# Kernel tuning notes

Measured on AMD Instinct MI355X. Metric: run time of the kernel, lower is better.

## Reference

```python
import jax, jax.numpy as jnp
import numpy as np

N, D, E, H, K = 16384, 256, 8, 512, 2


def setup_inputs() -> dict:
    key = jax.random.key(0)
    ks = jax.random.split(key, 5)
    inputs = jax.random.normal(ks[0], (N, D), dtype=jnp.float32)
    Wg = jax.random.normal(ks[1], (D, E), dtype=jnp.float32) * 0.05
    w1 = jax.random.normal(ks[2], (E, D, H), dtype=jnp.float32) * 0.05
    b1 = jnp.zeros((E, H), dtype=jnp.float32)
    w2 = jax.random.normal(ks[3], (E, H, D), dtype=jnp.float32) * 0.05
    b2 = jnp.zeros((E, D), dtype=jnp.float32)
    return {"inputs": inputs, "Wg": Wg, "w1": w1, "b1": b1, "w2": w2, "b2": b2}


def reference(inputs, Wg, w1, b1, w2, b2):
    # gate + top-k routing (softmax over the selected logits only, as in the torch code)
    gate_logits = inputs @ Wg                       # [N, E]
    topw, topi = jax.lax.top_k(gate_logits, K)      # [N, K]
    topw = jax.nn.softmax(topw.astype(jnp.float32), axis=1).astype(inputs.dtype)
    # combine weights scattered back into a dense [N, E] matrix (dispatch/combine)
    combine = jnp.zeros((N, E), dtype=inputs.dtype)
    combine = combine.at[jnp.arange(N)[:, None], topi].add(topw)  # [N, E]
    # expert MLP (Linear -> GELU(exact) -> Linear), computed per expert and
    # combined with the sparse routing weights (pool='sum')
    h = jax.nn.gelu(jnp.einsum('nd,edh->neh', inputs, w1) + b1[None], approximate=False)  # [N,E,H]
    y = jnp.einsum('neh,ehd->ned', h, w2) + b2[None]                                      # [N,E,D]
    return jnp.einsum('ne,ned->nd', combine, y)                                           # [N,D]
```

## Files before the change

### kernel.cpp

```cpp
#include <hip/hip_runtime.h>

#define NTOK 16384
#define DIM 256
#define NEXP 8
#define HID 512
#define CAP 5120
#define CSTRIDE 16

typedef unsigned short ushort_t;
typedef short bf16x8 __attribute__((ext_vector_type(8)));
typedef float f32x4 __attribute__((ext_vector_type(4)));

static __device__ __forceinline__ ushort_t f2bf(float f) {
    unsigned int u = __float_as_uint(f);
    unsigned int r = (u + 0x7FFFu + ((u >> 16) & 1u)) >> 16;
    return (ushort_t)r;
}
static __device__ __forceinline__ float bf2f(ushort_t u) {
    unsigned int x = ((unsigned int)u) << 16;
    return __uint_as_float(x);
}
static __device__ __forceinline__ float gelu_fast(float v) {
    float v2 = v * v;
    float u = v * __builtin_fmaf(v2, -0.1029407079f, -2.3022090196f);
    float e = __builtin_amdgcn_exp2f(u);
    return v * __builtin_amdgcn_rcpf(1.0f + e);
}

__global__ void k_prep(const float* __restrict__ X, const float* __restrict__ Wg,
                       const float* __restrict__ w1, const float* __restrict__ w2,
                       int* counts, int* tok_list, int* inv_idx, float* inv_w,
                       ushort_t* __restrict__ Xb,
                       ushort_t* __restrict__ w1t, ushort_t* __restrict__ w2t) {
    __shared__ __align__(16) char smem[69504];
    int tid = threadIdx.x;
    if (blockIdx.x >= 256) {
        ushort_t (*tile)[72] = (ushort_t(*)[72])smem;
        int b = blockIdx.x - 256;
        const float* src; ushort_t* dst; int R, C, e, t;
        if (b < 256) { e = b >> 5; t = b & 31; src = w1; dst = w1t + e * DIM * HID; R = DIM; C = HID; }
        else { b -= 256; e = b >> 5; t = b & 31; src = w2; dst = w2t + e * DIM * HID; R = HID; C = DIM; }
        size_t ebase = (size_t)e * DIM * HID;
        int tilesC = C >> 6;
        int rt = t / tilesC, ct = t % tilesC;
        for (int i = 0; i < 16; i++) {
            int flat = i * 256 + tid;
            int lr = flat >> 6, lc = flat & 63;
            tile[lr][lc] = f2bf(src[ebase + (size_t)(rt * 64 + lr) * C + ct * 64 + lc]);
        }
        __syncthreads();
        for (int i = 0; i < 16; i++) {
            int flat = i * 256 + tid;
            int lr = flat >> 6, lc = flat & 63;
            dst[(ct * 64 + lr) * R + rt * 64 + lc] = tile[lc][lr];
        }
        return;
    }
    float (*xs)[257] = (float(*)[257])smem;
    float (*lg)[8] = (float(*)[8])(smem + 65792);
    int* te0 = (int*)(smem + 67840);
    int* te1 = (int*)(smem + 68096);
    int* lo0 = (int*)(smem + 68352);
    int* lo1 = (int*)(smem + 68608);
    float* tw0 = (float*)(smem + 68864);
    float* tw1 = (float*)(smem + 69120);
    int* lcnt = (int*)(smem + 69376);
    int* gbase = (int*)(smem + 69408);
    int tok0 = blockIdx.x * 64;
    if (tid < NEXP) lcnt[tid] = 0;
    for (int i = 0; i < 8; i++) {
        int flat = i * 256 + tid;
        int r = flat >> 5, c8 = (flat & 31) << 3;
        const float* row = X + (size_t)(tok0 + r) * DIM + c8;
        float4 a = *(const float4*)row;
        float4 b = *(const float4*)(row + 4);
        xs[r][c8 + 0] = a.x; xs[r][c8 + 1] = a.y; xs[r][c8 + 2] = a.z; xs[r][c8 + 3] = a.w;
        xs[r][c8 + 4] = b.x; xs[r][c8 + 5] = b.y; xs[r][c8 + 6] = b.z; xs[r][c8 + 7] = b.w;
    }
    __syncthreads();
    for (int i = 0; i < 8; i++) {
        int flat = i * 256 + tid;
        int r = flat >> 5, c8 = (flat & 31) << 3;
        ushort_t pk[8];
#pragma unroll
        for (int j = 0; j < 8; j++) pk[j] = f2bf(xs[r][c8 + j]);
        *(int4*)(Xb + (size_t)(tok0 + r) * DIM + c8) = *(const int4*)pk;
    }
    int tl = tid & 63, pair = tid >> 6;
    float l0 = 0.f, l1 = 0.f;
    for (int d = 0; d < DIM; d++) {
        float x = xs[tl][d];
        l0 += x * Wg[d * NEXP + 2 * pair];
        l1 += x * Wg[d * NEXP + 2 * pair + 1];
    }
    lg[tl][2 * pair] = l0; lg[tl][2 * pair + 1] = l1;
    __syncthreads();
    if (tid < 64) {
        float best = -1e30f; int bi = 0;
#pragma unroll
        for (int e = 0; e < NEXP; e++) { float v = lg[tid][e]; if (v > best) { best = v; bi = e; } }
        float best2 = -1e30f; int bi2 = 0;
#pragma unroll
        for (int e = 0; e < NEXP; e++) { if (e == bi) continue; float v = lg[tid][e]; if (v > best2) { best2 = v; bi2 = e; } }
        float ed = __expf(best2 - best);
        te0[tid] = bi; te1[tid] = bi2;
        tw0[tid] = 1.0f / (1.0f + ed);
        tw1[tid] = ed / (1.0f + ed);
        lo0[tid] = atomicAdd(&lcnt[bi], 1);
        lo1[tid] = atomicAdd(&lcnt[bi2], 1);
    }
    __syncthreads();
    if (tid < NEXP) gbase[tid] = atomicAdd(&counts[tid * CSTRIDE], lcnt[tid]);
    __syncthreads();
    if (tid < 64) {
        int token = tok0 + tid;
        int e0 = te0[tid], e1 = te1[tid];
        int p0 = gbase[e0] + lo0[tid]; if (p0 >= CAP) p0 = CAP - 1;
        int p1 = gbase[e1] + lo1[tid]; if (p1 >= CAP) p1 = CAP - 1;
        tok_list[e0 * CAP + p0] = token;
        tok_list[e1 * CAP + p1] = token;
        inv_idx[token * 2]     = (e0 << 16) | p0;  inv_w[token * 2]     = tw0[tid];
        inv_idx[token * 2 + 1] = (e1 << 16) | p1;  inv_w[token * 2 + 1] = tw1[tid];
    }
}

__launch_bounds__(512, 4)
__global__ void k_mlp1(const ushort_t* __restrict__ Xb, const ushort_t* __restrict__ w1t,
                       const float* __restrict__ b1,
                       const int* __restrict__ counts, const int* __restrict__ tok_list,
                       ushort_t* __restrict__ hb) {
    __shared__ ushort_t B1[64 * 264];
    int b = blockIdx.x;
    int e = b / 320;
    int rem = b % 320;
    int hq = rem / 40, tile = rem % 40;
    int count = counts[e * CSTRIDE];
    if (count > CAP) count = CAP;
    int t0 = tile * 128;
    if (t0 >= count) return;

    int tid = threadIdx.x;
    int w = tid >> 6, l = tid & 63, ln = l & 15, q = l >> 4;

    const ushort_t* w1te = w1t + (size_t)e * DIM * HID + (size_t)hq * 64 * DIM;
#pragma unroll
    for (int i = 0; i < 4; i++) {
        int flat = i * 512 + tid;
        int hr = flat >> 5, c8 = (flat & 31) << 3;
        *(int4*)(B1 + hr * 264 + c8) = *(const int4*)(w1te + hr * DIM + c8);
    }
    int arow = t0 + 16 * w + ln;
    int ci = (arow < count) ? arow : (count - 1);
    int atok = tok_list[e * CAP + ci];
    const ushort_t* xrow = Xb + (size_t)atok * DIM;
    bf16x8 xf[8];
#pragma unroll
    for (int ks = 0; ks < 8; ks++)
        xf[ks] = *(const bf16x8*)(xrow + ks * 32 + q * 8);
    __syncthreads();

    f32x4 zf = {0.f, 0.f, 0.f, 0.f};
    f32x4 acc[4];
#pragma unroll
    for (int i = 0; i < 4; i++) acc[i] = zf;
#pragma unroll
    for (int ks = 0; ks < 8; ks++) {
        bf16x8 xk = xf[ks];
#pragma unroll
        for (int cf = 0; cf < 4; cf++) {
            bf16x8 wfr = *(const bf16x8*)(B1 + (cf * 16 + ln) * 264 + ks * 32 + q * 8);
            acc[cf] = __builtin_amdgcn_mfma_f32_16x16x32_bf16(wfr, xk, acc[cf], 0, 0, 0);
        }
    }
    size_t hrowbase = ((size_t)e * CAP + t0 + 16 * w + ln) * HID + hq * 64;
#pragma unroll
    for (int cf = 0; cf < 4; cf++) {
        float4 bv = *(const float4*)(b1 + e * HID + hq * 64 + cf * 16 + q * 4);
        ushort4 pk;
        pk.x = f2bf(gelu_fast(acc[cf][0] + bv.x));
        pk.y = f2bf(gelu_fast(acc[cf][1] + bv.y));
        pk.z = f2bf(gelu_fast(acc[cf][2] + bv.z));
        pk.w = f2bf(gelu_fast(acc[cf][3] + bv.w));
        *(ushort4*)(hb + hrowbase + cf * 16 + q * 4) = pk;
    }
}

__launch_bounds__(512, 2)
__global__ void k_mlp2(const ushort_t* __restrict__ hb, const ushort_t* __restrict__ w2t,
                       const float* __restrict__ b2,
                       const int* __restrict__ counts, ushort_t* __restrict__ yb) {
    __shared__ ushort_t B2[64 * 520];
    int b = blockIdx.x;
    int e = b / 160;
    int rem = b % 160;
    int dq = rem / 40, tile = rem % 40;
    int count = counts[e * CSTRIDE];
    if (count > CAP) count = CAP;
    int t0 = tile * 128;
    if (t0 >= count) return;

    int tid = threadIdx.x;
    int w = tid >> 6, l = tid & 63, ln = l & 15, q = l >> 4;

    const ushort_t* w2te = w2t + (size_t)e * DIM * HID + (size_t)dq * 64 * HID;
#pragma unroll
    for (int i = 0; i < 8; i++) {
        int flat = i * 512 + tid;
        int dr = flat >> 6, c8 = (flat & 63) << 3;
        *(int4*)(B2 + dr * 520 + c8) = *(const int4*)(w2te + dr * HID + c8);
    }
    int arow = t0 + 16 * w + ln;
    int ci = (arow < count) ? arow : (count - 1);
    const ushort_t* hrow = hb + ((size_t)e * CAP + ci) * HID;
    bf16x8 af[16];
#pragma unroll
    for (int ks = 0; ks < 16; ks++)
        af[ks] = *(const bf16x8*)(hrow + ks * 32 + q * 8);
    __syncthreads();

    f32x4 zf = {0.f, 0.f, 0.f, 0.f};
    f32x4 acc[4];
#pragma unroll
    for (int i = 0; i < 4; i++) acc[i] = zf;
#pragma unroll
    for (int ks = 0; ks < 16; ks++) {
        bf16x8 hk = af[ks];
#pragma unroll
        for (int cf = 0; cf < 4; cf++) {
            bf16x8 wfr = *(const bf16x8*)(B2 + (cf * 16 + ln) * 520 + ks * 32 + q * 8);
            acc[cf] = __builtin_amdgcn_mfma_f32_16x16x32_bf16(wfr, hk, acc[cf], 0, 0, 0);
        }
    }
    size_t yrowbase = ((size_t)e * CAP + t0 + 16 * w + ln) * DIM + dq * 64;
#pragma unroll
    for (int cf = 0; cf < 4; cf++) {
        float4 bv = *(const float4*)(b2 + e * DIM + dq * 64 + cf * 16 + q * 4);
        ushort4 pk;
        pk.x = f2bf(acc[cf][0] + bv.x);
        pk.y = f2bf(acc[cf][1] + bv.y);
        pk.z = f2bf(acc[cf][2] + bv.z);
        pk.w = f2bf(acc[cf][3] + bv.w);
        *(ushort4*)(yb + yrowbase + cf * 16 + q * 4) = pk;
    }
}

__global__ void k_combine(const ushort_t* __restrict__ yb, const int* __restrict__ inv_idx,
                          const float* __restrict__ inv_w, float* __restrict__ out) {
    int tid = threadIdx.x;
    int n = blockIdx.x * 8 + (tid >> 5);
    int l32 = tid & 31, c8 = l32 << 3;
    int i0 = inv_idx[2 * n], i1 = inv_idx[2 * n + 1];
    float w0 = inv_w[2 * n], w1 = inv_w[2 * n + 1];
    size_t r0 = (size_t)(i0 >> 16) * CAP + (i0 & 0xFFFF);
    size_t r1 = (size_t)(i1 >> 16) * CAP + (i1 & 0xFFFF);
    int4 v0 = *(const int4*)(yb + r0 * DIM + c8);
    int4 v1 = *(const int4*)(yb + r1 * DIM + c8);
    ushort_t* p0 = (ushort_t*)&v0;
    ushort_t* p1 = (ushort_t*)&v1;
    float4 oa, ob;
    oa.x = w0 * bf2f(p0[0]) + w1 * bf2f(p1[0]);
    oa.y = w0 * bf2f(p0[1]) + w1 * bf2f(p1[1]);
    oa.z = w0 * bf2f(p0[2]) + w1 * bf2f(p1[2]);
    oa.w = w0 * bf2f(p0[3]) + w1 * bf2f(p1[3]);
    ob.x = w0 * bf2f(p0[4]) + w1 * bf2f(p1[4]);
    ob.y = w0 * bf2f(p0[5]) + w1 * bf2f(p1[5]);
    ob.z = w0 * bf2f(p0[6]) + w1 * bf2f(p1[6]);
    ob.w = w0 * bf2f(p0[7]) + w1 * bf2f(p1[7]);
    float4* op = (float4*)(out + (size_t)n * DIM + c8);
    op[0] = oa; op[1] = ob;
}

extern "C" void kernel_launch(void* const* d_in, const int* in_sizes, int n_in,
                              void* d_out, int out_size, void* d_ws, size_t ws_size,
                              hipStream_t stream) {
    const float* X  = (const float*)d_in[0];
    const float* Wg = (const float*)d_in[1];
    const float* w1 = (const float*)d_in[2];
    const float* b1 = (const float*)d_in[3];
    const float* w2 = (const float*)d_in[4];
    const float* b2 = (const float*)d_in[5];

    char* ws = (char*)d_ws;
    size_t off = 0;
    int* counts = (int*)(ws + off);        off = 1024;
    int* tok_list = (int*)(ws + off);      off += (size_t)NEXP * CAP * 4;
    int* inv_idx = (int*)(ws + off);       off += (size_t)NTOK * 2 * 4;
    float* inv_w = (float*)(ws + off);     off += (size_t)NTOK * 2 * 4;
    ushort_t* w1t = (ushort_t*)(ws + off); off += (size_t)NEXP * DIM * HID * 2;
    ushort_t* w2t = (ushort_t*)(ws + off); off += (size_t)NEXP * DIM * HID * 2;
    ushort_t* Xb = (ushort_t*)(ws + off);  off += (size_t)NTOK * DIM * 2;
    ushort_t* hb = (ushort_t*)(ws + off);  off += (size_t)NEXP * CAP * HID * 2;
    ushort_t* yb = (ushort_t*)(ws + off);  off += (size_t)NEXP * CAP * DIM * 2;

    hipMemsetAsync(counts, 0, 1024, stream);
    k_prep<<<768, 256, 0, stream>>>(X, Wg, w1, w2, counts, tok_list, inv_idx, inv_w, Xb, w1t, w2t);
    k_mlp1<<<NEXP * 40 * 8, 512, 0, stream>>>(Xb, w1t, b1, counts, tok_list, hb);
    k_mlp2<<<NEXP * 40 * 4, 512, 0, stream>>>(hb, w2t, b2, counts, yb);
    k_combine<<<2048, 256, 0, stream>>>(yb, inv_idx, inv_w, (float*)d_out);
}
```

Measured before the change: 161.1 us.

## Halve block size and give each wave two 16-row token groups in MLP kernels

Both expert MLP kernels now launch 256 threads instead of 512, and each wave computes two 16-token row groups that share every LDS weight fragment load. This halves LDS weight reads per MFMA and doubles per-wave MFMA work. k_mlp2 splits its K loop into two halves so only 16 activation fragments per pass stay live, and both kernels now skip stores for rows beyond count. The costs are more register pressure per wave, fewer waves to cover the cooperative weight loads, and unchanged LDS footprint per block.

```diff
diff --git a/kernel.cpp b/kernel.cpp
--- a/kernel.cpp
+++ b/kernel.cpp
@@ -124,7 +124,7 @@
     }
 }
 
-__launch_bounds__(512, 4)
+__launch_bounds__(256, 4)
 __global__ void k_mlp1(const ushort_t* __restrict__ Xb, const ushort_t* __restrict__ w1t,
                        const float* __restrict__ b1,
                        const int* __restrict__ counts, const int* __restrict__ tok_list,
@@ -144,48 +144,60 @@
 
     const ushort_t* w1te = w1t + (size_t)e * DIM * HID + (size_t)hq * 64 * DIM;
 #pragma unroll
-    for (int i = 0; i < 4; i++) {
-        int flat = i * 512 + tid;
+    for (int i = 0; i < 8; i++) {
+        int flat = i * 256 + tid;
         int hr = flat >> 5, c8 = (flat & 31) << 3;
         *(int4*)(B1 + hr * 264 + c8) = *(const int4*)(w1te + hr * DIM + c8);
     }
-    int arow = t0 + 16 * w + ln;
-    int ci = (arow < count) ? arow : (count - 1);
-    int atok = tok_list[e * CAP + ci];
-    const ushort_t* xrow = Xb + (size_t)atok * DIM;
-    bf16x8 xf[8];
-#pragma unroll
-    for (int ks = 0; ks < 8; ks++)
-        xf[ks] = *(const bf16x8*)(xrow + ks * 32 + q * 8);
+    int arow0 = t0 + 32 * w + ln;
+    int arow1 = arow0 + 16;
+    int ci0 = (arow0 < count) ? arow0 : (count - 1);
+    int ci1 = (arow1 < count) ? arow1 : (count - 1);
+    const ushort_t* x0 = Xb + (size_t)tok_list[e * CAP + ci0] * DIM;
+    const ushort_t* x1 = Xb + (size_t)tok_list[e * CAP + ci1] * DIM;
+    bf16x8 xf[2][8];
+#pragma unroll
+    for (int ks = 0; ks < 8; ks++) {
+        xf[0][ks] = *(const bf16x8*)(x0 + ks * 32 + q * 8);
+        xf[1][ks] = *(const bf16x8*)(x1 + ks * 32 + q * 8);
+    }
     __syncthreads();
 
     f32x4 zf = {0.f, 0.f, 0.f, 0.f};
-    f32x4 acc[4];
-#pragma unroll
-    for (int i = 0; i < 4; i++) acc[i] = zf;
+    f32x4 acc[2][4];
+#pragma unroll
+    for (int tg = 0; tg < 2; tg++)
+#pragma unroll
+        for (int i = 0; i < 4; i++) acc[tg][i] = zf;
 #pragma unroll
     for (int ks = 0; ks < 8; ks++) {
-        bf16x8 xk = xf[ks];
 #pragma unroll
         for (int cf = 0; cf < 4; cf++) {
             bf16x8 wfr = *(const bf16x8*)(B1 + (cf * 16 + ln) * 264 + ks * 32 + q * 8);
-            acc[cf] = __builtin_amdgcn_mfma_f32_16x16x32_bf16(wfr, xk, acc[cf], 0, 0, 0);
-        }
-    }
-    size_t hrowbase = ((size_t)e * CAP + t0 + 16 * w + ln) * HID + hq * 64;
-#pragma unroll
-    for (int cf = 0; cf < 4; cf++) {
-        float4 bv = *(const float4*)(b1 + e * HID + hq * 64 + cf * 16 + q * 4);
-        ushort4 pk;
-        pk.x = f2bf(gelu_fast(acc[cf][0] + bv.x));
-        pk.y = f2bf(gelu_fast(acc[cf][1] + bv.y));
-        pk.z = f2bf(gelu_fast(acc[cf][2] + bv.z));
-        pk.w = f2bf(gelu_fast(acc[cf][3] + bv.w));
-        *(ushort4*)(hb + hrowbase + cf * 16 + q * 4) = pk;
-    }
-}
-
-__launch_bounds__(512, 2)
+            acc[0][cf] = __builtin_amdgcn_mfma_f32_16x16x32_bf16(wfr, xf[0][ks], acc[0][cf], 0, 0, 0);
+            acc[1][cf] = __builtin_amdgcn_mfma_f32_16x16x32_bf16(wfr, xf[1][ks], acc[1][cf], 0, 0, 0);
+        }
+    }
+#pragma unroll
+    for (int tg = 0; tg < 2; tg++) {
+        int arow = (tg == 0) ? arow0 : arow1;
+        if (arow < count) {
+            size_t hrowbase = ((size_t)e * CAP + arow) * HID + hq * 64;
+#pragma unroll
+            for (int cf = 0; cf < 4; cf++) {
+                float4 bv = *(const float4*)(b1 + e * HID + hq * 64 + cf * 16 + q * 4);
+                ushort4 pk;
+                pk.x = f2bf(gelu_fast(acc[tg][cf][0] + bv.x));
+                pk.y = f2bf(gelu_fast(acc[tg][cf][1] + bv.y));
+                pk.z = f2bf(gelu_fast(acc[tg][cf][2] + bv.z));
+                pk.w = f2bf(gelu_fast(acc[tg][cf][3] + bv.w));
+                *(ushort4*)(hb + hrowbase + cf * 16 + q * 4) = pk;
+            }
+        }
+    }
+}
+
+__launch_bounds__(256, 4)
 __global__ void k_mlp2(const ushort_t* __restrict__ hb, const ushort_t* __restrict__ w2t,
                        const float* __restrict__ b2,
                        const int* __restrict__ counts, ushort_t* __restrict__ yb) {
@@ -204,43 +216,59 @@
 
     const ushort_t* w2te = w2t + (size_t)e * DIM * HID + (size_t)dq * 64 * HID;
 #pragma unroll
-    for (int i = 0; i < 8; i++) {
-        int flat = i * 512 + tid;
+    for (int i = 0; i < 16; i++) {
+        int flat = i * 256 + tid;
         int dr = flat >> 6, c8 = (flat & 63) << 3;
         *(int4*)(B2 + dr * 520 + c8) = *(const int4*)(w2te + dr * HID + c8);
     }
-    int arow = t0 + 16 * w + ln;
-    int ci = (arow < count) ? arow : (count - 1);
-    const ushort_t* hrow = hb + ((size_t)e * CAP + ci) * HID;
-    bf16x8 af[16];
-#pragma unroll
-    for (int ks = 0; ks < 16; ks++)
-        af[ks] = *(const bf16x8*)(hrow + ks * 32 + q * 8);
+    int arow0 = t0 + 32 * w + ln;
+    int arow1 = arow0 + 16;
+    int ci0 = (arow0 < count) ? arow0 : (count - 1);
+    int ci1 = (arow1 < count) ? arow1 : (count - 1);
+    const ushort_t* h0 = hb + ((size_t)e * CAP + ci0) * HID;
+    const ushort_t* h1 = hb + ((size_t)e * CAP + ci1) * HID;
     __syncthreads();
 
     f32x4 zf = {0.f, 0.f, 0.f, 0.f};
-    f32x4 acc[4];
-#pragma unroll
-    for (int i = 0; i < 4; i++) acc[i] = zf;
-#pragma unroll
-    for (int ks = 0; ks < 16; ks++) {
-        bf16x8 hk = af[ks];
-#pragma unroll
-        for (int cf = 0; cf < 4; cf++) {
-            bf16x8 wfr = *(const bf16x8*)(B2 + (cf * 16 + ln) * 520 + ks * 32 + q * 8);
-            acc[cf] = __builtin_amdgcn_mfma_f32_16x16x32_bf16(wfr, hk, acc[cf], 0, 0, 0);
-        }
-    }
-    size_t yrowbase = ((size_t)e * CAP + t0 + 16 * w + ln) * DIM + dq * 64;
-#pragma unroll
-    for (int cf = 0; cf < 4; cf++) {
-        float4 bv = *(const float4*)(b2 + e * DIM + dq * 64 + cf * 16 + q * 4);
-        ushort4 pk;
-        pk.x = f2bf(acc[cf][0] + bv.x);
-        pk.y = f2bf(acc[cf][1] + bv.y);
-        pk.z = f2bf(acc[cf][2] + bv.z);
-        pk.w = f2bf(acc[cf][3] + bv.w);
-        *(ushort4*)(yb + yrowbase + cf * 16 + q * 4) = pk;
+    f32x4 acc[2][4];
+#pragma unroll
+    for (int tg = 0; tg < 2; tg++)
+#pragma unroll
+        for (int i = 0; i < 4; i++) acc[tg][i] = zf;
+#pragma unroll 1
+    for (int kh = 0; kh < 2; kh++) {
+        bf16x8 af[2][8];
+#pragma unroll
+        for (int ks = 0; ks < 8; ks++) {
+            af[0][ks] = *(const bf16x8*)(h0 + kh * 256 + ks * 32 + q * 8);
+            af[1][ks] = *(const bf16x8*)(h1 + kh * 256 + ks * 32 + q * 8);
+        }
+#pragma unroll
+        for (int ks = 0; ks < 8; ks++) {
+#pragma unroll
+            for (int cf = 0; cf < 4; cf++) {
+                bf16x8 wfr = *(const bf16x8*)(B2 + (cf * 16 + ln) * 520 + kh * 256 + ks * 32 + q * 8);
+                acc[0][cf] = __builtin_amdgcn_mfma_f32_16x16x32_bf16(wfr, af[0][ks], acc[0][cf], 0, 0, 0);
+                acc[1][cf] = __builtin_amdgcn_mfma_f32_16x16x32_bf16(wfr, af[1][ks], acc[1][cf], 0, 0, 0);
+            }
+        }
+    }
+#pragma unroll
+    for (int tg = 0; tg < 2; tg++) {
+        int arow = (tg == 0) ? arow0 : arow1;
+        if (arow < count) {
+            size_t yrowbase = ((size_t)e * CAP + arow) * DIM + dq * 64;
+#pragma unroll
+            for (int cf = 0; cf < 4; cf++) {
+                float4 bv = *(const float4*)(b2 + e * DIM + dq * 64 + cf * 16 + q * 4);
+                ushort4 pk;
+                pk.x = f2bf(acc[tg][cf][0] + bv.x);
+                pk.y = f2bf(acc[tg][cf][1] + bv.y);
+                pk.z = f2bf(acc[tg][cf][2] + bv.z);
+                pk.w = f2bf(acc[tg][cf][3] + bv.w);
+                *(ushort4*)(yb + yrowbase + cf * 16 + q * 4) = pk;
+            }
+        }
     }
 }
 
@@ -294,7 +322,7 @@
 
     hipMemsetAsync(counts, 0, 1024, stream);
     k_prep<<<768, 256, 0, stream>>>(X, Wg, w1, w2, counts, tok_list, inv_idx, inv_w, Xb, w1t, w2t);
-    k_mlp1<<<NEXP * 40 * 8, 512, 0, stream>>>(Xb, w1t, b1, counts, tok_list, hb);
-    k_mlp2<<<NEXP * 40 * 4, 512, 0, stream>>>(hb, w2t, b2, counts, yb);
+    k_mlp1<<<NEXP * 40 * 8, 256, 0, stream>>>(Xb, w1t, b1, counts, tok_list, hb);
+    k_mlp2<<<NEXP * 40 * 4, 256, 0, stream>>>(hb, w2t, b2, counts, yb);
     k_combine<<<2048, 256, 0, stream>>>(yb, inv_idx, inv_w, (float*)d_out);
 }
```

New measurement: 166.0 us. +3.1%, slower.
